# Kernel optimization log

Measured on AMD Instinct MI355X. Metric: run time of the kernel, lower is better.

Reference implementation:

```python
import jax, jax.numpy as jnp
import numpy as np

B, T, U, H, M, K, C = 64, 800, 80, 512, 20, 10, 80  # batch, tsteps, char len, rnn_size, nmixtures, kmixtures, char_vec_len


def _lstm(x, W, Uw, b):
    """Keras-semantics LSTM (gate order i,f,g,o), zero initial state. x: [B,T,D] -> [B,T,H]."""
    xg = jnp.einsum('btd,dh->bth', x, W) + b  # precompute input contribution
    h0 = jnp.zeros((x.shape[0], Uw.shape[0]), x.dtype)
    c0 = jnp.zeros_like(h0)

    def step(carry, zt):
        h, c = carry
        z = zt + h @ Uw
        i, f, g, o = jnp.split(z, 4, axis=-1)
        c = jax.nn.sigmoid(f) * c + jax.nn.sigmoid(i) * jnp.tanh(g)
        h = jax.nn.sigmoid(o) * jnp.tanh(c)
        return (h, c), h

    _, hs = jax.lax.scan(step, (h0, c0), jnp.swapaxes(xg, 0, 1))
    return jnp.swapaxes(hs, 0, 1)


def _forward(stroke_data, char_seq, kappa0, W0, U0, b0, W1, U1, b1, W2, U2, b2, Wa, ba, Wm, bm):
    lstm0_out = _lstm(stroke_data, W0, U0, b0)  # [B,T,H]
    # Attention window: the per-timestep loop in the source only carries kappa,
    # which is a running sum of exp(kappa_offset) -> vectorize via cumsum.
    abk = jnp.exp(jnp.einsum('bth,hk->btk', lstm0_out, Wa) + ba)  # [B,T,3K]
    alpha, beta, koff = jnpp_split = jnp.split(abk, 3, axis=-1)
    kappa = kappa0[:, None, :, 0] + jnp.cumsum(koff, axis=1)  # [B,T,K]
    u = jnp.arange(char_seq.shape[1], dtype=stroke_data.dtype)  # [U]
    # phi: [B,T,U] = sum_k alpha * exp(-beta * (kappa - u)^2)
    phi = jnp.sum(alpha[..., None] * jnp.exp(-beta[..., None] * (kappa[..., None] - u) ** 2), axis=2)
    windows = jnp.einsum('btu,buc->btc', phi, char_seq)  # [B,T,C]
    aug = jnp.concatenate([lstm0_out, windows, stroke_data], axis=-1)
    lstm1_out = _lstm(aug, W1, U1, b1)
    lstm2_out = _lstm(lstm1_out, W2, U2, b2)
    mdn = jnp.einsum('bth,hn->btn', lstm2_out, Wm) + bm  # [B,T,1+6M]
    eos_hat = mdn[..., 0:1]
    pi_hat, mu1, mu2, s1_hat, s2_hat, rho_hat = jnp.split(mdn[..., 1:], 6, axis=-1)
    return jnp.concatenate([
        jax.nn.sigmoid(-eos_hat),
        jax.nn.softmax(pi_hat, axis=-1),
        mu1, mu2,
        jnp.exp(s1_hat), jnp.exp(s2_hat),
        jnp.tanh(rho_hat),
    ], axis=-1)  # [B,T,1+6M]


def setup_inputs() -> dict:
    key = jax.random.key(0)
    ks = jax.random.split(key, 12)
    init = lambda k, shape: jax.random.truncated_normal(k, -2.0, 2.0, shape, jnp.float32) * 0.075
    return {
        'stroke_data': jax.random.normal(ks[0], (B, T, 3), jnp.float32),
        'char_seq': jax.nn.one_hot(jax.random.randint(ks[1], (B, U), 0, C), C, dtype=jnp.float32),
        'kappa0': jnp.zeros((B, K, 1), jnp.float32),
        'W0': init(ks[2], (3, 4 * H)), 'U0': init(ks[3], (H, 4 * H)), 'b0': jnp.zeros((4 * H,)),
        'W1': init(ks[4], (H + C + 3, 4 * H)), 'U1': init(ks[5], (H, 4 * H)), 'b1': jnp.zeros((4 * H,)),
        'W2': init(ks[6], (H, 4 * H)), 'U2': init(ks[7], (H, 4 * H)), 'b2': jnp.zeros((4 * H,)),
        'Wa': init(ks[8], (H, 3 * K)),
        'ba': -3.0 + 0.25 * jax.random.truncated_normal(ks[9], -2.0, 2.0, (3 * K,), jnp.float32),
        'Wm': init(ks[10], (H, 1 + 6 * M)), 'bm': jnp.zeros((1 + 6 * M,)),
    }


def reference(stroke_data, char_seq, kappa0, W0, U0, b0, W1, U1, b1, W2, U2, b2, Wa, ba, Wm, bm):
    return _forward(stroke_data, char_seq, kappa0, W0, U0, b0, W1, U1, b1, W2, U2, b2, Wa, ba, Wm, bm)
```

## Files before the change

kernel.cpp:

```cpp
#include <hip/hip_runtime.h>

typedef unsigned short u16;
typedef unsigned int u32;
typedef short v8s __attribute__((ext_vector_type(8)));
typedef float v4f __attribute__((ext_vector_type(4)));
typedef unsigned int v4u __attribute__((ext_vector_type(4)));
typedef unsigned int v2u __attribute__((ext_vector_type(2)));

#define MFMA16 __builtin_amdgcn_mfma_f32_16x16x32_bf16

constexpr int TT = 800;
constexpr int NBLK = 178;

constexpr int AUGB  = 2240;
constexpr int AUG2B = 2048;

constexpr size_t AUGR_OFF  = 131072;
constexpr size_t AUG2R_OFF = AUGR_OFF + (size_t)4 * 64 * AUGB;
constexpr size_t WAT_OFF   = AUG2R_OFF + (size_t)4 * 64 * AUG2B;
constexpr size_t WS_ZERO   = WAT_OFF + (size_t)32 * 512 * 2;

constexpr u32 SMEM_BYTES = 82944;

enum { G_S0D = 0, G_SAD = 1, G_S1D = 2, G_S2D = 3, G_S1R = 4, G_SAR = 5, G_S2R = 6, G_SMR = 7 };

__device__ __forceinline__ float bf2f(u16 u) { return __uint_as_float(((u32)u) << 16); }
__device__ __forceinline__ u16 f2bf(float f) {
    u32 x = __float_as_uint(f);
    return (u16)((x + 0x7fffu + ((x >> 16) & 1u)) >> 16);
}
__device__ __forceinline__ short f2bfs(float f) { return (short)f2bf(f); }
__device__ __forceinline__ float sigf(float x) { return 1.f / (1.f + __expf(-x)); }
__device__ __forceinline__ float tanhf2(float x) { return 1.f - 2.f / (1.f + __expf(2.f * x)); }

__device__ __forceinline__ __amdgpu_buffer_rsrc_t mkrsrc(const void* p) {
    return __builtin_amdgcn_make_buffer_rsrc((void*)p, (short)0, -1, 0x00020000);
}
__device__ __forceinline__ v4u ldu4(__amdgpu_buffer_rsrc_t r, int off) {
    return __builtin_amdgcn_raw_buffer_load_b128(r, off, 0, 17);
}
__device__ __forceinline__ void stq8(__amdgpu_buffer_rsrc_t r, int off, u16 a, u16 b, u16 c, u16 d) {
    v2u t; t[0] = (u32)a | ((u32)b << 16); t[1] = (u32)c | ((u32)d << 16);
    __builtin_amdgcn_raw_buffer_store_b64(t, r, off, 0, 17);
}
__device__ __forceinline__ void stq4(__amdgpu_buffer_rsrc_t r, int off, u16 a, u16 b) {
    u32 t = (u32)a | ((u32)b << 16);
    __builtin_amdgcn_raw_buffer_store_b32(t, r, off, 0, 17);
}

__device__ __forceinline__ void publish(u32* ctrl, int g, int t, int blk) {
    __hip_atomic_fetch_add(ctrl + g * 4096 + (t & 3) * 1024 + (blk & 15) * 64, 1u,
                           __ATOMIC_RELAXED, __HIP_MEMORY_SCOPE_AGENT);
}
__device__ __forceinline__ void wait4(u32* ctrl,
    int g0, int t0, u32 n0, int g1, int t1, u32 n1,
    int g2, int t2, u32 n2, int g3, int t3, u32 n3)
{
    if (threadIdx.x < 64) {
        const int lane = threadIdx.x;
        const int cl = lane >> 4, k = lane & 15;
        int g, tt; u32 nn;
        if (cl == 0)      { g = g0; tt = t0; nn = n0; }
        else if (cl == 1) { g = g1; tt = t1; nn = n1; }
        else if (cl == 2) { g = g2; tt = t2; nn = n2; }
        else              { g = g3; tt = t3; nn = n3; }
        const u32 tgt = (g >= 0 && tt >= 0) ? nn * (u32)((tt >> 2) + 1) : 0u;
        u32* p = (tgt > 0) ? (ctrl + g * 4096 + (tt & 3) * 1024 + k * 64) : (u32*)0;
        int sp = 0;
        for (;;) {
            u32 v = p ? __hip_atomic_load(p, __ATOMIC_RELAXED, __HIP_MEMORY_SCOPE_AGENT) : 0u;
            v += __shfl_xor(v, 1); v += __shfl_xor(v, 2);
            v += __shfl_xor(v, 4); v += __shfl_xor(v, 8);
            const bool bad = (tgt > 0) && (v < tgt);
            if (__ballot(bad) == 0ull) break;
            if (sp >= 2) __builtin_amdgcn_s_sleep(4);
            else if (sp == 1) __builtin_amdgcn_s_sleep(1);
            sp++;
        }
    }
    __syncthreads();
}

__global__ void wat_init(const float* __restrict__ Wa, u16* __restrict__ WaT) {
    __amdgpu_buffer_rsrc_t r = mkrsrc(WaT);
    for (int idx = blockIdx.x * 256 + threadIdx.x; idx < 32 * 512 / 2; idx += gridDim.x * 256) {
        const int e0 = idx * 2, e1 = e0 + 1;
        const int n0 = e0 >> 9, k0 = e0 & 511;
        const int n1 = e1 >> 9, k1 = e1 & 511;
        const u16 a = (n0 < 30) ? f2bf(Wa[k0 * 30 + n0]) : (u16)0;
        const u16 b = (n1 < 30) ? f2bf(Wa[k1 * 30 + n1]) : (u16)0;
        stq4(r, idx * 4, a, b);
    }
}

__global__ __launch_bounds__(256, 1) void hw_main(
    const float* __restrict__ stroke, const float* __restrict__ charseq, const float* __restrict__ kappa0,
    const float* __restrict__ W0, const float* __restrict__ U0, const float* __restrict__ b0,
    const float* __restrict__ W1, const float* __restrict__ U1, const float* __restrict__ b1,
    const float* __restrict__ W2, const float* __restrict__ U2, const float* __restrict__ b2,
    const float* __restrict__ ba, const float* __restrict__ Wm, const float* __restrict__ bm,
    float* __restrict__ out, char* __restrict__ ws)
{
    extern __shared__ __align__(16) char smem[];
    u32* ctrl = (u32*)ws;
    u16* augr  = (u16*)(ws + AUGR_OFF);
    u16* aug2r = (u16*)(ws + AUG2R_OFF);
    const u16* WaT = (const u16*)(ws + WAT_OFF);

    const int blk = blockIdx.x, tid = threadIdx.x;
    const int wave = tid >> 6, lane = tid & 63;
    const int quad = lane >> 4, l15 = lane & 15;

    if (blk < 32) {
        const int cs = blk & 15, mg = blk >> 4;
        __amdgpu_buffer_rsrc_t ra = mkrsrc(augr);
        u16*   aL  = (u16*)smem;
        float* zb  = (float*)(smem + 33280);
        float* w0s = (float*)(smem + 50176);
        float* b0s = (float*)(smem + 51712);
        if (tid < 128) {
            const int cn2 = (tid >> 5) * 512 + cs * 32 + (tid & 31);
            b0s[tid] = b0[cn2];
            #pragma unroll
            for (int d = 0; d < 3; d++) w0s[d * 128 + tid] = W0[d * 2048 + cn2];
        }
        v8s bw0[16], bw1[16];
        {
            const int cnA = wave * 512 + cs * 32 + l15;
            const int cnB = cnA + 16;
            #pragma unroll
            for (int kc = 0; kc < 16; kc++)
                #pragma unroll
                for (int j = 0; j < 8; j++) {
                    const int k = kc * 32 + quad * 8 + j;
                    bw0[kc][j] = f2bfs(U0[k * 2048 + cnA]);
                    bw1[kc][j] = f2bfs(U0[k * 2048 + cnB]);
                }
        }
        float cst[4] = {0.f, 0.f, 0.f, 0.f};
        __syncthreads();
        #pragma unroll 1
        for (int t = 0; t < TT; t++) {
            wait4(ctrl, G_S0D, t - 1, 32, G_S1R, t - 4, 64, G_SAR, t - 4, 16, -1, 0, 0);
            {
                const int base = (((t + 3) & 3) * 64 + mg * 32) * AUGB;
                #pragma unroll
                for (int c8 = 0; c8 < 8; c8++) {
                    const int c = tid + 256 * c8;
                    const int row = c >> 6, off = c & 63;
                    v4u d = ldu4(ra, base + row * AUGB + off * 16);
                    *(v4u*)((char*)aL + row * 1040 + off * 16) = d;
                }
            }
            __syncthreads();
            v4f c0a = {0,0,0,0}, c0b = {0,0,0,0}, c1a = {0,0,0,0}, c1b = {0,0,0,0};
            const int xo = quad * 16;
            #pragma unroll
            for (int kc = 0; kc < 16; kc++) {
                v8s x0 = *(const v8s*)((const char*)aL + l15 * 1040 + kc * 64 + xo);
                v8s x1 = *(const v8s*)((const char*)aL + (16 + l15) * 1040 + kc * 64 + xo);
                c0a = MFMA16(x0, bw0[kc], c0a, 0, 0, 0);
                c1a = MFMA16(x0, bw1[kc], c1a, 0, 0, 0);
                c0b = MFMA16(x1, bw0[kc], c0b, 0, 0, 0);
                c1b = MFMA16(x1, bw1[kc], c1b, 0, 0, 0);
            }
            const int n0 = wave * 32 + l15, n1 = n0 + 16;
            #pragma unroll
            for (int r = 0; r < 4; r++) {
                zb[(quad * 4 + r) * 132 + n0] = c0a[r];
                zb[(quad * 4 + r) * 132 + n1] = c1a[r];
                zb[(16 + quad * 4 + r) * 132 + n0] = c0b[r];
                zb[(16 + quad * 4 + r) * 132 + n1] = c1b[r];
            }
            __syncthreads();
            {
                const int bl = tid & 31, jj = tid >> 5;
                const int b = mg * 32 + bl;
                const float xx0 = stroke[(b * TT + t) * 3 + 0];
                const float xx1 = stroke[(b * TT + t) * 3 + 1];
                const float xx2 = stroke[(b * TT + t) * 3 + 2];
                u16 hv[4];
                #pragma unroll
                for (int m = 0; m < 4; m++) {
                    const int j = jj * 4 + m;
                    float z[4];
                    #pragma unroll
                    for (int g = 0; g < 4; g++) {
                        const int n = g * 32 + j;
                        z[g] = zb[bl * 132 + n] + b0s[n] + xx0 * w0s[n] + xx1 * w0s[128 + n] + xx2 * w0s[256 + n];
                    }
                    const float cc = sigf(z[1]) * cst[m] + sigf(z[0]) * tanhf2(z[2]);
                    cst[m] = cc;
                    hv[m] = f2bf(sigf(z[3]) * tanhf2(cc));
                }
                stq8(ra, ((t & 3) * 64 + b) * AUGB + (cs * 32 + jj * 4) * 2, hv[0], hv[1], hv[2], hv[3]);
            }
            __syncthreads();
            if (tid == 0) publish(ctrl, G_S0D, t, blk);
        }
    } else if (blk < 96) {
        const int q = blk - 32, cs = q >> 1, mg = q & 1;
        __amdgpu_buffer_rsrc_t ra = mkrsrc(augr);
        __amdgpu_buffer_rsrc_t r2 = mkrsrc(aug2r);
        u16*   aL  = (u16*)smem;
        float* zb  = (float*)(smem + 72192);
        float* b1s = (float*)(smem + 80896);
        if (tid < 64) b1s[tid] = b1[(tid >> 4) * 512 + cs * 16 + (tid & 15)];
        v8s bw[35];
        {
            const int cn = wave * 512 + cs * 16 + l15;
            #pragma unroll
            for (int kc = 0; kc < 35; kc++)
                #pragma unroll
                for (int j = 0; j < 8; j++) {
                    const int k = kc * 32 + quad * 8 + j;
                    short v = 0;
                    if (k < 595) v = f2bfs(W1[k * 2048 + cn]);
                    else if (k >= 596 && k < 1108) v = f2bfs(U1[(k - 596) * 2048 + cn]);
                    bw[kc][j] = v;
                }
        }
        float cst[2] = {0.f, 0.f};
        __syncthreads();
        #pragma unroll 1
        for (int t = 0; t < TT; t++) {
            wait4(ctrl, G_S0D, t, 32, G_SAD, t, 16, G_S1D, t - 1, 64, G_S2R, t - 4, 64);
            {
                const int base = ((t & 3) * 64 + mg * 32) * AUGB;
                #pragma unroll
                for (int c18 = 0; c18 < 18; c18++) {
                    const int c = tid + 256 * c18;
                    if (c < 4480) {
                        const int row = c / 140, off = c - row * 140;
                        v4u d = ldu4(ra, base + row * AUGB + off * 16);
                        *(v4u*)((char*)aL + row * 2256 + off * 16) = d;
                    }
                }
            }
            __syncthreads();
            if (tid == 0) publish(ctrl, G_S1R, t, blk);
            v4f c0 = {0,0,0,0}, c1 = {0,0,0,0};
            const int xo = quad * 16;
            #pragma unroll
            for (int kc = 0; kc < 35; kc++) {
                v8s x0 = *(const v8s*)((const char*)aL + l15 * 2256 + kc * 64 + xo);
                v8s x1 = *(const v8s*)((const char*)aL + (16 + l15) * 2256 + kc * 64 + xo);
                c0 = MFMA16(x0, bw[kc], c0, 0, 0, 0);
                c1 = MFMA16(x1, bw[kc], c1, 0, 0, 0);
            }
            #pragma unroll
            for (int r = 0; r < 4; r++) {
                zb[(quad * 4 + r) * 68 + wave * 17 + l15] = c0[r];
                zb[(16 + quad * 4 + r) * 68 + wave * 17 + l15] = c1[r];
            }
            __syncthreads();
            {
                const int bl = tid & 31, jj = tid >> 5;
                const int b = mg * 32 + bl;
                u16 hv[2];
                #pragma unroll
                for (int m = 0; m < 2; m++) {
                    const int j = jj * 2 + m;
                    float z[4];
                    #pragma unroll
                    for (int g = 0; g < 4; g++)
                        z[g] = zb[bl * 68 + g * 17 + j] + b1s[g * 16 + j];
                    const float cc = sigf(z[1]) * cst[m] + sigf(z[0]) * tanhf2(z[2]);
                    cst[m] = cc;
                    hv[m] = f2bf(sigf(z[3]) * tanhf2(cc));
                }
                stq4(ra, (((t + 1) & 3) * 64 + b) * AUGB + (596 + cs * 16 + jj * 2) * 2, hv[0], hv[1]);
                stq4(r2, ((t & 3) * 64 + b) * AUG2B + (cs * 16 + jj * 2) * 2, hv[0], hv[1]);
            }
            __syncthreads();
            if (tid == 0) publish(ctrl, G_S1D, t, blk);
        }
    } else if (blk < 160) {
        const int q = blk - 96, cs = q >> 1, mg = q & 1;
        __amdgpu_buffer_rsrc_t r2 = mkrsrc(aug2r);
        u16*   aL  = (u16*)smem;
        float* zb  = (float*)(smem + 66048);
        float* b2s = (float*)(smem + 74752);
        if (tid < 64) b2s[tid] = b2[(tid >> 4) * 512 + cs * 16 + (tid & 15)];
        v8s bw[32];
        {
            const int cn = wave * 512 + cs * 16 + l15;
            #pragma unroll
            for (int kc = 0; kc < 32; kc++)
                #pragma unroll
                for (int j = 0; j < 8; j++) {
                    const int k = kc * 32 + quad * 8 + j;
                    bw[kc][j] = (k < 512) ? f2bfs(W2[k * 2048 + cn]) : f2bfs(U2[(k - 512) * 2048 + cn]);
                }
        }
        float cst[2] = {0.f, 0.f};
        __syncthreads();
        #pragma unroll 1
        for (int t = 0; t < TT; t++) {
            wait4(ctrl, G_S1D, t, 64, G_S2D, t - 1, 64, G_SMR, t - 4, 2, -1, 0, 0);
            {
                const int base = ((t & 3) * 64 + mg * 32) * AUG2B;
                #pragma unroll
                for (int c16 = 0; c16 < 16; c16++) {
                    const int c = tid + 256 * c16;
                    const int row = c >> 7, off = c & 127;
                    v4u d = ldu4(r2, base + row * AUG2B + off * 16);
                    *(v4u*)((char*)aL + row * 2064 + off * 16) = d;
                }
            }
            __syncthreads();
            if (tid == 0) publish(ctrl, G_S2R, t, blk);
            v4f c0 = {0,0,0,0}, c1 = {0,0,0,0};
            const int xo = quad * 16;
            #pragma unroll
            for (int kc = 0; kc < 32; kc++) {
                v8s x0 = *(const v8s*)((const char*)aL + l15 * 2064 + kc * 64 + xo);
                v8s x1 = *(const v8s*)((const char*)aL + (16 + l15) * 2064 + kc * 64 + xo);
                c0 = MFMA16(x0, bw[kc], c0, 0, 0, 0);
                c1 = MFMA16(x1, bw[kc], c1, 0, 0, 0);
            }
            #pragma unroll
            for (int r = 0; r < 4; r++) {
                zb[(quad * 4 + r) * 68 + wave * 17 + l15] = c0[r];
                zb[(16 + quad * 4 + r) * 68 + wave * 17 + l15] = c1[r];
            }
            __syncthreads();
            {
                const int bl = tid & 31, jj = tid >> 5;
                const int b = mg * 32 + bl;
                u16 hv[2];
                #pragma unroll
                for (int m = 0; m < 2; m++) {
                    const int j = jj * 2 + m;
                    float z[4];
                    #pragma unroll
                    for (int g = 0; g < 4; g++)
                        z[g] = zb[bl * 68 + g * 17 + j] + b2s[g * 16 + j];
                    const float cc = sigf(z[1]) * cst[m] + sigf(z[0]) * tanhf2(z[2]);
                    cst[m] = cc;
                    hv[m] = f2bf(sigf(z[3]) * tanhf2(cc));
                }
                stq4(r2, (((t + 1) & 3) * 64 + b) * AUG2B + (512 + cs * 16 + jj * 2) * 2, hv[0], hv[1]);
            }
            __syncthreads();
            if (tid == 0) publish(ctrl, G_S2D, t, blk);
        }
    } else if (blk < 176) {
        const int a = blk - 160;
        const int b = a * 4 + wave;
        __amdgpu_buffer_rsrc_t ra = mkrsrc(augr);
        u16*   watl = (u16*)smem;
        u16*   hrow = (u16*)(smem + 33280);
        float* phis = (float*)(smem + 37440);
        u16*   idxs = (u16*)(smem + 38720);
        {
            #pragma unroll
            for (int c8 = 0; c8 < 8; c8++) {
                const int c = tid + 256 * c8;
                const int row = c >> 6, off = c & 63;
                *(v4u*)((char*)watl + row * 1040 + off * 16) = *(const v4u*)(WaT + row * 512 + off * 8);
            }
        }
        #pragma unroll
        for (int rep = 0; rep < 2; rep++) {
            const int u = rep * 64 + lane;
            if (u < 80) {
                int c = 0;
                #pragma unroll 1
                for (int cc = 0; cc < 80; cc++)
                    if (charseq[b * 6400 + u * 80 + cc] > 0.5f) c = cc;
                idxs[wave * 80 + u] = (u16)c;
            }
        }
        float kap = (lane < 10) ? kappa0[b * 10 + lane] : 0.f;
        const float baf = (lane < 30) ? ba[lane] : 0.f;
        const int nn = lane & 31;
        const int k0 = (lane >> 5) * 256;
        const u16* wrow = watl + nn * 520 + k0;
        __syncthreads();
        #pragma unroll 1
        for (int t = 0; t < TT; t++) {
            wait4(ctrl, G_S0D, t, 32, G_S1R, t - 4, 64, -1, 0, 0, -1, 0, 0);
            {
                const int row = tid >> 6, off = tid & 63;
                v4u d = ldu4(ra, ((t & 3) * 64 + a * 4 + row) * AUGB + off * 16);
                *(v4u*)((char*)hrow + row * 1040 + off * 16) = d;
            }
            __syncthreads();
            if (tid == 0) publish(ctrl, G_SAR, t, blk);
            float acc = 0.f;
            #pragma unroll
            for (int kk = 0; kk < 32; kk++) {
                v8s hv = *(const v8s*)((const char*)hrow + wave * 1040 + (k0 + kk * 8) * 2);
                v8s wv = *(const v8s*)(wrow + kk * 8);
                #pragma unroll
                for (int e = 0; e < 8; e++) acc += bf2f((u16)hv[e]) * bf2f((u16)wv[e]);
            }
            acc += __shfl_xor(acc, 32);
            const float abk = __expf(acc + baf);
            const float kofv = __shfl(abk, 20 + (lane < 10 ? lane : 0));
            if (lane < 10) kap += kofv;
            const float u1f = (float)lane;
            float p1 = 0.f, p2 = 0.f;
            #pragma unroll
            for (int kk = 0; kk < 10; kk++) {
                const float al = __shfl(abk, kk);
                const float be = __shfl(abk, 10 + kk);
                const float kp = __shfl(kap, kk);
                const float d1 = kp - u1f, d2 = kp - (u1f + 64.f);
                p1 += al * __expf(-be * d1 * d1);
                p2 += al * __expf(-be * d2 * d2);
            }
            phis[wave * 80 + lane] = p1;
            if (lane < 16) phis[wave * 80 + 64 + lane] = p2;
            __syncthreads();
            const int db = (((t & 3) * 64 + b) * AUGB) + 512 * 2;
            if (lane < 40) {
                const int c0 = 2 * lane;
                float w0 = 0.f, w1 = 0.f;
                #pragma unroll 1
                for (int u = 0; u < 80; u++) {
                    const float pv = phis[wave * 80 + u];
                    const int ix = (int)idxs[wave * 80 + u];
                    w0 += (ix == c0)     ? pv : 0.f;
                    w1 += (ix == c0 + 1) ? pv : 0.f;
                }
                stq4(ra, db + c0 * 2, f2bf(w0), f2bf(w1));
            } else if (lane == 40) {
                stq4(ra, db + 80 * 2, f2bf(stroke[(b * TT + t) * 3 + 0]), f2bf(stroke[(b * TT + t) * 3 + 1]));
            } else if (lane == 41) {
                stq4(ra, db + 82 * 2, f2bf(stroke[(b * TT + t) * 3 + 2]), (u16)0);
            }
            __syncthreads();
            if (tid == 0) publish(ctrl, G_SAD, t, blk);
        }
    } else {
        const int mgs = blk - 176;
        __amdgpu_buffer_rsrc_t r2 = mkrsrc(aug2r);
        u16*   aL = (u16*)smem;
        float* zb = (float*)(smem + 33280);
        v8s bw0[16], bw1[16];
        {
            const int nA = wave * 32 + l15, nB = nA + 16;
            #pragma unroll
            for (int kc = 0; kc < 16; kc++)
                #pragma unroll
                for (int j = 0; j < 8; j++) {
                    const int k = kc * 32 + quad * 8 + j;
                    bw0[kc][j] = (nA < 121) ? f2bfs(Wm[k * 121 + nA]) : (short)0;
                    bw1[kc][j] = (nB < 121) ? f2bfs(Wm[k * 121 + nB]) : (short)0;
                }
        }
        __syncthreads();
        #pragma unroll 1
        for (int t = 0; t < TT; t++) {
            wait4(ctrl, G_S2D, t, 64, -1, 0, 0, -1, 0, 0, -1, 0, 0);
            {
                const int base = (((t + 1) & 3) * 64 + mgs * 32) * AUG2B + 1024;
                #pragma unroll
                for (int c8 = 0; c8 < 8; c8++) {
                    const int c = tid + 256 * c8;
                    const int row = c >> 6, off = c & 63;
                    v4u d = ldu4(r2, base + row * AUG2B + off * 16);
                    *(v4u*)((char*)aL + row * 1040 + off * 16) = d;
                }
            }
            __syncthreads();
            if (tid == 0) publish(ctrl, G_SMR, t, blk);
            v4f c0a = {0,0,0,0}, c0b = {0,0,0,0}, c1a = {0,0,0,0}, c1b = {0,0,0,0};
            const int xo = quad * 16;
            #pragma unroll
            for (int kc = 0; kc < 16; kc++) {
                v8s x0 = *(const v8s*)((const char*)aL + l15 * 1040 + kc * 64 + xo);
                v8s x1 = *(const v8s*)((const char*)aL + (16 + l15) * 1040 + kc * 64 + xo);
                c0a = MFMA16(x0, bw0[kc], c0a, 0, 0, 0);
                c1a = MFMA16(x0, bw1[kc], c1a, 0, 0, 0);
                c0b = MFMA16(x1, bw0[kc], c0b, 0, 0, 0);
                c1b = MFMA16(x1, bw1[kc], c1b, 0, 0, 0);
            }
            const int n0 = wave * 32 + l15, n1 = n0 + 16;
            #pragma unroll
            for (int r = 0; r < 4; r++) {
                zb[(quad * 4 + r) * 132 + n0] = c0a[r];
                zb[(quad * 4 + r) * 132 + n1] = c1a[r];
                zb[(16 + quad * 4 + r) * 132 + n0] = c0b[r];
                zb[(16 + quad * 4 + r) * 132 + n1] = c1b[r];
            }
            __syncthreads();
            {
                const int b8 = tid >> 3, g8 = tid & 7;
                const int b = mgs * 32 + b8;
                const float* zr = zb + b8 * 132;
                float* orow = out + ((size_t)(b * TT + t)) * 121;
                if (g8 == 0) {
                    orow[0] = sigf(-(zr[0] + bm[0]));
                    float mx = -1e30f;
                    float zv[20];
                    #pragma unroll 1
                    for (int nl = 1; nl <= 20; nl++) { zv[nl - 1] = zr[nl] + bm[nl]; mx = fmaxf(mx, zv[nl - 1]); }
                    float ss = 0.f;
                    #pragma unroll 1
                    for (int nl = 0; nl < 20; nl++) { zv[nl] = __expf(zv[nl] - mx); ss += zv[nl]; }
                    const float inv = 1.f / ss;
                    #pragma unroll 1
                    for (int nl = 0; nl < 20; nl++) orow[nl + 1] = zv[nl] * inv;
                } else if (g8 <= 2) {
                    const int s0 = 21 + (g8 - 1) * 20;
                    #pragma unroll 1
                    for (int nl = s0; nl < s0 + 20; nl++) orow[nl] = zr[nl] + bm[nl];
                } else if (g8 <= 4) {
                    const int s0 = 61 + (g8 - 3) * 20;
                    #pragma unroll 1
                    for (int nl = s0; nl < s0 + 20; nl++) orow[nl] = __expf(zr[nl] + bm[nl]);
                } else if (g8 <= 6) {
                    const int s0 = 101 + (g8 - 5) * 10;
                    #pragma unroll 1
                    for (int nl = s0; nl < s0 + 10; nl++) orow[nl] = tanhf2(zr[nl] + bm[nl]);
                }
            }
            __syncthreads();
        }
    }
}

extern "C" void kernel_launch(void* const* d_in, const int* in_sizes, int n_in,
                              void* d_out, int out_size, void* d_ws, size_t ws_size,
                              hipStream_t stream) {
    const float* stroke  = (const float*)d_in[0];
    const float* charseq = (const float*)d_in[1];
    const float* kappa0  = (const float*)d_in[2];
    const float* W0 = (const float*)d_in[3];
    const float* U0 = (const float*)d_in[4];
    const float* b0 = (const float*)d_in[5];
    const float* W1 = (const float*)d_in[6];
    const float* U1 = (const float*)d_in[7];
    const float* b1 = (const float*)d_in[8];
    const float* W2 = (const float*)d_in[9];
    const float* U2 = (const float*)d_in[10];
    const float* b2 = (const float*)d_in[11];
    const float* Wa = (const float*)d_in[12];
    const float* ba = (const float*)d_in[13];
    const float* Wm = (const float*)d_in[14];
    const float* bm = (const float*)d_in[15];
    char* ws = (char*)d_ws;

    static bool attr_done = false;
    if (!attr_done) {
        hipFuncSetAttribute((const void*)hw_main,
                            hipFuncAttributeMaxDynamicSharedMemorySize, SMEM_BYTES);
        attr_done = true;
    }

    hipMemsetAsync(d_ws, 0, WS_ZERO, stream);
    wat_init<<<8, 256, 0, stream>>>(Wa, (u16*)(ws + WAT_OFF));
    hw_main<<<NBLK, 256, SMEM_BYTES, stream>>>(stroke, charseq, kappa0, W0, U0, b0,
                                               W1, U1, b1, W2, U2, b2, ba, Wm, bm,
                                               (float*)d_out, ws);
}
```

Baseline: 8.759 ms.

## Merge pairs of persistent blocks into 512-thread blocks, halving grid size

Each persistent role block now runs 8 waves instead of 4 and owns twice as many gate columns (or both batch halves for the MDN stage), so the grid shrinks from 178 to 89 blocks. This halves the number of blocks that publish and poll the inter-block step counters, which is meant to cut synchronization latency per timestep. In exchange each block does more LDS staging and the intra-block barriers cover twice the waves. The __launch_bounds__(512,2) hint may also limit registers for the large weight-resident register arrays and cause spills.

Result: slower. 9.900 ms (+13.0%).

```diff
diff --git a/kernel.cpp b/kernel.cpp
--- a/kernel.cpp
+++ b/kernel.cpp
@@ -10,7 +10,7 @@
 #define MFMA16 __builtin_amdgcn_mfma_f32_16x16x32_bf16
 
 constexpr int TT = 800;
-constexpr int NBLK = 178;
+constexpr int NBLK = 89;
 
 constexpr int AUGB  = 2240;
 constexpr int AUG2B = 2048;
@@ -20,7 +20,7 @@
 constexpr size_t WAT_OFF   = AUG2R_OFF + (size_t)4 * 64 * AUG2B;
 constexpr size_t WS_ZERO   = WAT_OFF + (size_t)32 * 512 * 2;
 
-constexpr u32 SMEM_BYTES = 82944;
+constexpr u32 SMEM_BYTES = 100352;
 
 enum { G_S0D = 0, G_SAD = 1, G_S1D = 2, G_S2D = 3, G_S1R = 4, G_SAR = 5, G_S2R = 6, G_SMR = 7 };
 
@@ -93,7 +93,7 @@
     }
 }
 
-__global__ __launch_bounds__(256, 1) void hw_main(
+__global__ __launch_bounds__(512, 2) void hw_main(
     const float* __restrict__ stroke, const float* __restrict__ charseq, const float* __restrict__ kappa0,
     const float* __restrict__ W0, const float* __restrict__ U0, const float* __restrict__ b0,
     const float* __restrict__ W1, const float* __restrict__ U1, const float* __restrict__ b1,
@@ -111,22 +111,24 @@
     const int wave = tid >> 6, lane = tid & 63;
     const int quad = lane >> 4, l15 = lane & 15;
 
-    if (blk < 32) {
-        const int cs = blk & 15, mg = blk >> 4;
+    if (blk < 16) {
+        const int cs = blk & 7, mg = blk >> 3;
+        const int gw = wave & 3, sw = wave >> 2;
         __amdgpu_buffer_rsrc_t ra = mkrsrc(augr);
         u16*   aL  = (u16*)smem;
         float* zb  = (float*)(smem + 33280);
-        float* w0s = (float*)(smem + 50176);
-        float* b0s = (float*)(smem + 51712);
-        if (tid < 128) {
-            const int cn2 = (tid >> 5) * 512 + cs * 32 + (tid & 31);
+        float* w0s = (float*)(smem + 66560);
+        float* b0s = (float*)(smem + 69632);
+        if (tid < 256) {
+            const int gg = tid >> 6, j = tid & 63;
+            const int cn2 = gg * 512 + cs * 64 + j;
             b0s[tid] = b0[cn2];
             #pragma unroll
-            for (int d = 0; d < 3; d++) w0s[d * 128 + tid] = W0[d * 2048 + cn2];
+            for (int d = 0; d < 3; d++) w0s[d * 256 + tid] = W0[d * 2048 + cn2];
         }
         v8s bw0[16], bw1[16];
         {
-            const int cnA = wave * 512 + cs * 32 + l15;
+            const int cnA = gw * 512 + cs * 64 + sw * 32 + l15;
             const int cnB = cnA + 16;
             #pragma unroll
             for (int kc = 0; kc < 16; kc++)
@@ -141,12 +143,12 @@
         __syncthreads();
         #pragma unroll 1
         for (int t = 0; t < TT; t++) {
-            wait4(ctrl, G_S0D, t - 1, 32, G_S1R, t - 4, 64, G_SAR, t - 4, 16, -1, 0, 0);
+            wait4(ctrl, G_S0D, t - 1, 16, G_S1R, t - 4, 32, G_SAR, t - 4, 8, -1, 0, 0);
             {
                 const int base = (((t + 3) & 3) * 64 + mg * 32) * AUGB;
                 #pragma unroll
-                for (int c8 = 0; c8 < 8; c8++) {
-                    const int c = tid + 256 * c8;
+                for (int c4 = 0; c4 < 4; c4++) {
+                    const int c = tid + 512 * c4;
                     const int row = c >> 6, off = c & 63;
                     v4u d = ldu4(ra, base + row * AUGB + off * 16);
                     *(v4u*)((char*)aL + row * 1040 + off * 16) = d;
@@ -167,10 +169,10 @@
             const int n0 = wave * 32 + l15, n1 = n0 + 16;
             #pragma unroll
             for (int r = 0; r < 4; r++) {
-                zb[(quad * 4 + r) * 132 + n0] = c0a[r];
-                zb[(quad * 4 + r) * 132 + n1] = c1a[r];
-                zb[(16 + quad * 4 + r) * 132 + n0] = c0b[r];
-                zb[(16 + quad * 4 + r) * 132 + n1] = c1b[r];
+                zb[(quad * 4 + r) * 260 + n0] = c0a[r];
+                zb[(quad * 4 + r) * 260 + n1] = c1a[r];
+                zb[(16 + quad * 4 + r) * 260 + n0] = c0b[r];
+                zb[(16 + quad * 4 + r) * 260 + n1] = c1b[r];
             }
             __syncthreads();
             {
@@ -185,30 +187,33 @@
                     const int j = jj * 4 + m;
                     float z[4];
                     #pragma unroll
-                    for (int g = 0; g < 4; g++) {
-                        const int n = g * 32 + j;
-                        z[g] = zb[bl * 132 + n] + b0s[n] + xx0 * w0s[n] + xx1 * w0s[128 + n] + xx2 * w0s[256 + n];
+                    for (int gg = 0; gg < 4; gg++) {
+                        const int zn = ((j >> 5) * 4 + gg) * 32 + (j & 31);
+                        const int nb = gg * 64 + j;
+                        z[gg] = zb[bl * 260 + zn] + b0s[nb]
+                              + xx0 * w0s[nb] + xx1 * w0s[256 + nb] + xx2 * w0s[512 + nb];
                     }
                     const float cc = sigf(z[1]) * cst[m] + sigf(z[0]) * tanhf2(z[2]);
                     cst[m] = cc;
                     hv[m] = f2bf(sigf(z[3]) * tanhf2(cc));
                 }
-                stq8(ra, ((t & 3) * 64 + b) * AUGB + (cs * 32 + jj * 4) * 2, hv[0], hv[1], hv[2], hv[3]);
+                stq8(ra, ((t & 3) * 64 + b) * AUGB + (cs * 64 + jj * 4) * 2, hv[0], hv[1], hv[2], hv[3]);
             }
             __syncthreads();
             if (tid == 0) publish(ctrl, G_S0D, t, blk);
         }
-    } else if (blk < 96) {
-        const int q = blk - 32, cs = q >> 1, mg = q & 1;
+    } else if (blk < 48) {
+        const int q = blk - 16, cs = q >> 1, mg = q & 1;
+        const int gw = wave & 3, sw = wave >> 2;
         __amdgpu_buffer_rsrc_t ra = mkrsrc(augr);
         __amdgpu_buffer_rsrc_t r2 = mkrsrc(aug2r);
         u16*   aL  = (u16*)smem;
         float* zb  = (float*)(smem + 72192);
-        float* b1s = (float*)(smem + 80896);
-        if (tid < 64) b1s[tid] = b1[(tid >> 4) * 512 + cs * 16 + (tid & 15)];
+        float* b1s = (float*)(smem + 90112);
+        if (tid < 128) b1s[tid] = b1[(tid >> 5) * 512 + cs * 32 + (tid & 31)];
         v8s bw[35];
         {
-            const int cn = wave * 512 + cs * 16 + l15;
+            const int cn = gw * 512 + cs * 32 + sw * 16 + l15;
             #pragma unroll
             for (int kc = 0; kc < 35; kc++)
                 #pragma unroll
@@ -224,12 +229,12 @@
         __syncthreads();
         #pragma unroll 1
         for (int t = 0; t < TT; t++) {
-            wait4(ctrl, G_S0D, t, 32, G_SAD, t, 16, G_S1D, t - 1, 64, G_S2R, t - 4, 64);
+            wait4(ctrl, G_S0D, t, 16, G_SAD, t, 8, G_S1D, t - 1, 32, G_S2R, t - 4, 32);
             {
                 const int base = ((t & 3) * 64 + mg * 32) * AUGB;
                 #pragma unroll
-                for (int c18 = 0; c18 < 18; c18++) {
-                    const int c = tid + 256 * c18;
+                for (int c9 = 0; c9 < 9; c9++) {
+                    const int c = tid + 512 * c9;
                     if (c < 4480) {
                         const int row = c / 140, off = c - row * 140;
                         v4u d = ldu4(ra, base + row * AUGB + off * 16);
@@ -250,8 +255,8 @@
             }
             #pragma unroll
             for (int r = 0; r < 4; r++) {
-                zb[(quad * 4 + r) * 68 + wave * 17 + l15] = c0[r];
-                zb[(16 + quad * 4 + r) * 68 + wave * 17 + l15] = c1[r];
+                zb[(quad * 4 + r) * 140 + wave * 17 + l15] = c0[r];
+                zb[(16 + quad * 4 + r) * 140 + wave * 17 + l15] = c1[r];
             }
             __syncthreads();
             {
@@ -263,28 +268,29 @@
                     const int j = jj * 2 + m;
                     float z[4];
                     #pragma unroll
-                    for (int g = 0; g < 4; g++)
-                        z[g] = zb[bl * 68 + g * 17 + j] + b1s[g * 16 + j];
+                    for (int gg = 0; gg < 4; gg++)
+                        z[gg] = zb[bl * 140 + ((j >> 4) * 4 + gg) * 17 + (j & 15)] + b1s[gg * 32 + j];
                     const float cc = sigf(z[1]) * cst[m] + sigf(z[0]) * tanhf2(z[2]);
                     cst[m] = cc;
                     hv[m] = f2bf(sigf(z[3]) * tanhf2(cc));
                 }
-                stq4(ra, (((t + 1) & 3) * 64 + b) * AUGB + (596 + cs * 16 + jj * 2) * 2, hv[0], hv[1]);
-                stq4(r2, ((t & 3) * 64 + b) * AUG2B + (cs * 16 + jj * 2) * 2, hv[0], hv[1]);
+                stq4(ra, (((t + 1) & 3) * 64 + b) * AUGB + (596 + cs * 32 + jj * 2) * 2, hv[0], hv[1]);
+                stq4(r2, ((t & 3) * 64 + b) * AUG2B + (cs * 32 + jj * 2) * 2, hv[0], hv[1]);
             }
             __syncthreads();
             if (tid == 0) publish(ctrl, G_S1D, t, blk);
         }
-    } else if (blk < 160) {
-        const int q = blk - 96, cs = q >> 1, mg = q & 1;
+    } else if (blk < 80) {
+        const int q = blk - 48, cs = q >> 1, mg = q & 1;
+        const int gw = wave & 3, sw = wave >> 2;
         __amdgpu_buffer_rsrc_t r2 = mkrsrc(aug2r);
         u16*   aL  = (u16*)smem;
         float* zb  = (float*)(smem + 66048);
-        float* b2s = (float*)(smem + 74752);
-        if (tid < 64) b2s[tid] = b2[(tid >> 4) * 512 + cs * 16 + (tid & 15)];
+        float* b2s = (float*)(smem + 83968);
+        if (tid < 128) b2s[tid] = b2[(tid >> 5) * 512 + cs * 32 + (tid & 31)];
         v8s bw[32];
         {
-            const int cn = wave * 512 + cs * 16 + l15;
+            const int cn = gw * 512 + cs * 32 + sw * 16 + l15;
             #pragma unroll
             for (int kc = 0; kc < 32; kc++)
                 #pragma unroll
@@ -297,12 +303,12 @@
         __syncthreads();
         #pragma unroll 1
         for (int t = 0; t < TT; t++) {
-            wait4(ctrl, G_S1D, t, 64, G_S2D, t - 1, 64, G_SMR, t - 4, 2, -1, 0, 0);
+            wait4(ctrl, G_S1D, t, 32, G_S2D, t - 1, 32, G_SMR, t - 4, 1, -1, 0, 0);
             {
                 const int base = ((t & 3) * 64 + mg * 32) * AUG2B;
                 #pragma unroll
-                for (int c16 = 0; c16 < 16; c16++) {
-                    const int c = tid + 256 * c16;
+                for (int c8 = 0; c8 < 8; c8++) {
+                    const int c = tid + 512 * c8;
                     const int row = c >> 7, off = c & 127;
                     v4u d = ldu4(r2, base + row * AUG2B + off * 16);
                     *(v4u*)((char*)aL + row * 2064 + off * 16) = d;
@@ -321,8 +327,8 @@
             }
             #pragma unroll
             for (int r = 0; r < 4; r++) {
-                zb[(quad * 4 + r) * 68 + wave * 17 + l15] = c0[r];
-                zb[(16 + quad * 4 + r) * 68 + wave * 17 + l15] = c1[r];
+                zb[(quad * 4 + r) * 140 + wave * 17 + l15] = c0[r];
+                zb[(16 + quad * 4 + r) * 140 + wave * 17 + l15] = c1[r];
             }
             __syncthreads();
             {
@@ -334,29 +340,29 @@
                     const int j = jj * 2 + m;
                     float z[4];
                     #pragma unroll
-                    for (int g = 0; g < 4; g++)
-                        z[g] = zb[bl * 68 + g * 17 + j] + b2s[g * 16 + j];
+                    for (int gg = 0; gg < 4; gg++)
+                        z[gg] = zb[bl * 140 + ((j >> 4) * 4 + gg) * 17 + (j & 15)] + b2s[gg * 32 + j];
                     const float cc = sigf(z[1]) * cst[m] + sigf(z[0]) * tanhf2(z[2]);
                     cst[m] = cc;
                     hv[m] = f2bf(sigf(z[3]) * tanhf2(cc));
                 }
-                stq4(r2, (((t + 1) & 3) * 64 + b) * AUG2B + (512 + cs * 16 + jj * 2) * 2, hv[0], hv[1]);
+                stq4(r2, (((t + 1) & 3) * 64 + b) * AUG2B + (512 + cs * 32 + jj * 2) * 2, hv[0], hv[1]);
             }
             __syncthreads();
             if (tid == 0) publish(ctrl, G_S2D, t, blk);
         }
-    } else if (blk < 176) {
-        const int a = blk - 160;
-        const int b = a * 4 + wave;
+    } else if (blk < 88) {
+        const int a = blk - 80;
+        const int b = a * 8 + wave;
         __amdgpu_buffer_rsrc_t ra = mkrsrc(augr);
         u16*   watl = (u16*)smem;
         u16*   hrow = (u16*)(smem + 33280);
-        float* phis = (float*)(smem + 37440);
-        u16*   idxs = (u16*)(smem + 38720);
+        float* phis = (float*)(smem + 41600);
+        u16*   idxs = (u16*)(smem + 44160);
         {
             #pragma unroll
-            for (int c8 = 0; c8 < 8; c8++) {
-                const int c = tid + 256 * c8;
+            for (int c4 = 0; c4 < 4; c4++) {
+                const int c = tid + 512 * c4;
                 const int row = c >> 6, off = c & 63;
                 *(v4u*)((char*)watl + row * 1040 + off * 16) = *(const v4u*)(WaT + row * 512 + off * 8);
             }
@@ -380,10 +386,10 @@
         __syncthreads();
         #pragma unroll 1
         for (int t = 0; t < TT; t++) {
-            wait4(ctrl, G_S0D, t, 32, G_S1R, t - 4, 64, -1, 0, 0, -1, 0, 0);
+            wait4(ctrl, G_S0D, t, 16, G_S1R, t - 4, 32, -1, 0, 0, -1, 0, 0);
             {
                 const int row = tid >> 6, off = tid & 63;
-                v4u d = ldu4(ra, ((t & 3) * 64 + a * 4 + row) * AUGB + off * 16);
+                v4u d = ldu4(ra, ((t & 3) * 64 + a * 8 + row) * AUGB + off * 16);
                 *(v4u*)((char*)hrow + row * 1040 + off * 16) = d;
             }
             __syncthreads();
@@ -435,13 +441,13 @@
             if (tid == 0) publish(ctrl, G_SAD, t, blk);
         }
     } else {
-        const int mgs = blk - 176;
+        const int mgs = wave >> 2, wv = wave & 3;
         __amdgpu_buffer_rsrc_t r2 = mkrsrc(aug2r);
         u16*   aL = (u16*)smem;
-        float* zb = (float*)(smem + 33280);
+        float* zb = (float*)(smem + 66560);
         v8s bw0[16], bw1[16];
         {
-            const int nA = wave * 32 + l15, nB = nA + 16;
+            const int nA = wv * 32 + l15, nB = nA + 16;
             #pragma unroll
             for (int kc = 0; kc < 16; kc++)
                 #pragma unroll
@@ -454,12 +460,12 @@
         __syncthreads();
         #pragma unroll 1
         for (int t = 0; t < TT; t++) {
-            wait4(ctrl, G_S2D, t, 64, -1, 0, 0, -1, 0, 0, -1, 0, 0);
-            {
-                const int base = (((t + 1) & 3) * 64 + mgs * 32) * AUG2B + 1024;
+            wait4(ctrl, G_S2D, t, 32, -1, 0, 0, -1, 0, 0, -1, 0, 0);
+            {
+                const int base = (((t + 1) & 3) * 64) * AUG2B + 1024;
                 #pragma unroll
                 for (int c8 = 0; c8 < 8; c8++) {
-                    const int c = tid + 256 * c8;
+                    const int c = tid + 512 * c8;
                     const int row = c >> 6, off = c & 63;
                     v4u d = ldu4(r2, base + row * AUG2B + off * 16);
                     *(v4u*)((char*)aL + row * 1040 + off * 16) = d;
@@ -471,25 +477,25 @@
             const int xo = quad * 16;
             #pragma unroll
             for (int kc = 0; kc < 16; kc++) {
-                v8s x0 = *(const v8s*)((const char*)aL + l15 * 1040 + kc * 64 + xo);
-                v8s x1 = *(const v8s*)((const char*)aL + (16 + l15) * 1040 + kc * 64 + xo);
+                v8s x0 = *(const v8s*)((const char*)aL + (mgs * 32 + l15) * 1040 + kc * 64 + xo);
+                v8s x1 = *(const v8s*)((const char*)aL + (mgs * 32 + 16 + l15) * 1040 + kc * 64 + xo);
                 c0a = MFMA16(x0, bw0[kc], c0a, 0, 0, 0);
                 c1a = MFMA16(x0, bw1[kc], c1a, 0, 0, 0);
                 c0b = MFMA16(x1, bw0[kc], c0b, 0, 0, 0);
                 c1b = MFMA16(x1, bw1[kc], c1b, 0, 0, 0);
             }
-            const int n0 = wave * 32 + l15, n1 = n0 + 16;
+            const int n0 = wv * 32 + l15, n1 = n0 + 16;
             #pragma unroll
             for (int r = 0; r < 4; r++) {
-                zb[(quad * 4 + r) * 132 + n0] = c0a[r];
-                zb[(quad * 4 + r) * 132 + n1] = c1a[r];
-                zb[(16 + quad * 4 + r) * 132 + n0] = c0b[r];
-                zb[(16 + quad * 4 + r) * 132 + n1] = c1b[r];
+                zb[(mgs * 32 + quad * 4 + r) * 132 + n0] = c0a[r];
+                zb[(mgs * 32 + quad * 4 + r) * 132 + n1] = c1a[r];
+                zb[(mgs * 32 + 16 + quad * 4 + r) * 132 + n0] = c0b[r];
+                zb[(mgs * 32 + 16 + quad * 4 + r) * 132 + n1] = c1b[r];
             }
             __syncthreads();
             {
                 const int b8 = tid >> 3, g8 = tid & 7;
-                const int b = mgs * 32 + b8;
+                const int b = b8;
                 const float* zr = zb + b8 * 132;
                 float* orow = out + ((size_t)(b * TT + t)) * 121;
                 if (g8 == 0) {
@@ -553,7 +559,7 @@
 
     hipMemsetAsync(d_ws, 0, WS_ZERO, stream);
     wat_init<<<8, 256, 0, stream>>>(Wa, (u16*)(ws + WAT_OFF));
-    hw_main<<<NBLK, 256, SMEM_BYTES, stream>>>(stroke, charseq, kappa0, W0, U0, b0,
+    hw_main<<<NBLK, 512, SMEM_BYTES, stream>>>(stroke, charseq, kappa0, W0, U0, b0,
                                                W1, U1, b1, W2, U2, b2, ba, Wm, bm,
                                                (float*)d_out, ws);
 }
```

## Split LSTM input waits per batch-half and overlap input-part MFMA with recurrent wait

Applied to the files above, without the earlier changes.

Synchronisation counters are now partitioned by batch half (mb offset), so each stage waits only on producers for its own 32-row batch group instead of all blocks. LSTM1 and LSTM2 blocks first load and multiply the input (lower-layer) part of their concatenated input, then wait on the previous-step recurrent hidden state before loading and multiplying the recurrent half. This moves the recurrent dependency later in each step. Stroke loads are hoisted ahead of the wait. The cost is an extra wait and barrier per step, and a risk of miscounting if the per-half counter targets are wrong.

Result: no change. 8.748 ms (-0.1%).

```diff
diff --git a/kernel.cpp b/kernel.cpp
--- a/kernel.cpp
+++ b/kernel.cpp
@@ -39,6 +39,9 @@
 __device__ __forceinline__ v4u ldu4(__amdgpu_buffer_rsrc_t r, int off) {
     return __builtin_amdgcn_raw_buffer_load_b128(r, off, 0, 17);
 }
+__device__ __forceinline__ v2u ldu8(__amdgpu_buffer_rsrc_t r, int off) {
+    return __builtin_amdgcn_raw_buffer_load_b64(r, off, 0, 17);
+}
 __device__ __forceinline__ void stq8(__amdgpu_buffer_rsrc_t r, int off, u16 a, u16 b, u16 c, u16 d) {
     v2u t; t[0] = (u32)a | ((u32)b << 16); t[1] = (u32)c | ((u32)d << 16);
     __builtin_amdgcn_raw_buffer_store_b64(t, r, off, 0, 17);
@@ -48,24 +51,24 @@
     __builtin_amdgcn_raw_buffer_store_b32(t, r, off, 0, 17);
 }
 
-__device__ __forceinline__ void publish(u32* ctrl, int g, int t, int blk) {
-    __hip_atomic_fetch_add(ctrl + g * 4096 + (t & 3) * 1024 + (blk & 15) * 64, 1u,
+__device__ __forceinline__ void publish(u32* ctrl, int g, int t, int sub) {
+    __hip_atomic_fetch_add(ctrl + g * 4096 + (t & 3) * 1024 + (sub & 15) * 64, 1u,
                            __ATOMIC_RELAXED, __HIP_MEMORY_SCOPE_AGENT);
 }
 __device__ __forceinline__ void wait4(u32* ctrl,
-    int g0, int t0, u32 n0, int g1, int t1, u32 n1,
-    int g2, int t2, u32 n2, int g3, int t3, u32 n3)
+    int g0, int t0, u32 n0, int m0, int g1, int t1, u32 n1, int m1,
+    int g2, int t2, u32 n2, int m2, int g3, int t3, u32 n3, int m3)
 {
     if (threadIdx.x < 64) {
         const int lane = threadIdx.x;
         const int cl = lane >> 4, k = lane & 15;
-        int g, tt; u32 nn;
-        if (cl == 0)      { g = g0; tt = t0; nn = n0; }
-        else if (cl == 1) { g = g1; tt = t1; nn = n1; }
-        else if (cl == 2) { g = g2; tt = t2; nn = n2; }
-        else              { g = g3; tt = t3; nn = n3; }
+        int g, tt, mb; u32 nn;
+        if (cl == 0)      { g = g0; tt = t0; nn = n0; mb = m0; }
+        else if (cl == 1) { g = g1; tt = t1; nn = n1; mb = m1; }
+        else if (cl == 2) { g = g2; tt = t2; nn = n2; mb = m2; }
+        else              { g = g3; tt = t3; nn = n3; mb = m3; }
         const u32 tgt = (g >= 0 && tt >= 0) ? nn * (u32)((tt >> 2) + 1) : 0u;
-        u32* p = (tgt > 0) ? (ctrl + g * 4096 + (tt & 3) * 1024 + k * 64) : (u32*)0;
+        u32* p = (tgt > 0) ? (ctrl + g * 4096 + (tt & 3) * 1024 + (mb + (k & 7)) * 64) : (u32*)0;
         int sp = 0;
         for (;;) {
             u32 v = p ? __hip_atomic_load(p, __ATOMIC_RELAXED, __HIP_MEMORY_SCOPE_AGENT) : 0u;
@@ -113,6 +116,7 @@
 
     if (blk < 32) {
         const int cs = blk & 15, mg = blk >> 4;
+        const int mb = mg * 8, sub = mb + (cs & 7);
         __amdgpu_buffer_rsrc_t ra = mkrsrc(augr);
         u16*   aL  = (u16*)smem;
         float* zb  = (float*)(smem + 33280);
@@ -138,10 +142,15 @@
                 }
         }
         float cst[4] = {0.f, 0.f, 0.f, 0.f};
+        const int bl_ = tid & 31;
+        const int bpre = mg * 32 + bl_;
         __syncthreads();
         #pragma unroll 1
         for (int t = 0; t < TT; t++) {
-            wait4(ctrl, G_S0D, t - 1, 32, G_S1R, t - 4, 64, G_SAR, t - 4, 16, -1, 0, 0);
+            const float xx0 = stroke[(bpre * TT + t) * 3 + 0];
+            const float xx1 = stroke[(bpre * TT + t) * 3 + 1];
+            const float xx2 = stroke[(bpre * TT + t) * 3 + 2];
+            wait4(ctrl, G_S0D, t - 1, 32, mb, G_S1R, t - 4, 64, mb, G_SAR, t - 4, 16, mb, -1, 0, 0, 0);
             {
                 const int base = (((t + 3) & 3) * 64 + mg * 32) * AUGB;
                 #pragma unroll
@@ -176,9 +185,6 @@
             {
                 const int bl = tid & 31, jj = tid >> 5;
                 const int b = mg * 32 + bl;
-                const float xx0 = stroke[(b * TT + t) * 3 + 0];
-                const float xx1 = stroke[(b * TT + t) * 3 + 1];
-                const float xx2 = stroke[(b * TT + t) * 3 + 2];
                 u16 hv[4];
                 #pragma unroll
                 for (int m = 0; m < 4; m++) {
@@ -196,10 +202,11 @@
                 stq8(ra, ((t & 3) * 64 + b) * AUGB + (cs * 32 + jj * 4) * 2, hv[0], hv[1], hv[2], hv[3]);
             }
             __syncthreads();
-            if (tid == 0) publish(ctrl, G_S0D, t, blk);
+            if (tid == 0) publish(ctrl, G_S0D, t, sub);
         }
     } else if (blk < 96) {
         const int q = blk - 32, cs = q >> 1, mg = q & 1;
+        const int mb = mg * 8, sub = mb + (cs & 7);
         __amdgpu_buffer_rsrc_t ra = mkrsrc(augr);
         __amdgpu_buffer_rsrc_t r2 = mkrsrc(aug2r);
         u16*   aL  = (u16*)smem;
@@ -220,29 +227,53 @@
                     bw[kc][j] = v;
                 }
         }
+        if (tid < 32) { v4u z4 = {0,0,0,0}; *(v4u*)((char*)aL + tid * 2256 + 2224) = z4; }
         float cst[2] = {0.f, 0.f};
         __syncthreads();
         #pragma unroll 1
         for (int t = 0; t < TT; t++) {
-            wait4(ctrl, G_S0D, t, 32, G_SAD, t, 16, G_S1D, t - 1, 64, G_S2R, t - 4, 64);
+            wait4(ctrl, G_S0D, t, 32, mb, G_SAD, t, 16, mb, G_S2R, t - 4, 64, mb, -1, 0, 0, 0);
             {
                 const int base = ((t & 3) * 64 + mg * 32) * AUGB;
                 #pragma unroll
-                for (int c18 = 0; c18 < 18; c18++) {
-                    const int c = tid + 256 * c18;
-                    if (c < 4480) {
-                        const int row = c / 140, off = c - row * 140;
+                for (int c10 = 0; c10 < 10; c10++) {
+                    const int c = tid + 256 * c10;
+                    if (c < 2400) {
+                        const int row = c / 75, off = c - row * 75;
                         v4u d = ldu4(ra, base + row * AUGB + off * 16);
                         *(v4u*)((char*)aL + row * 2256 + off * 16) = d;
                     }
                 }
             }
             __syncthreads();
-            if (tid == 0) publish(ctrl, G_S1R, t, blk);
+            if (tid == 0) publish(ctrl, G_S1R, t, sub);
+            wait4(ctrl, G_S1D, t - 1, 64, mb, -1, 0, 0, 0, -1, 0, 0, 0, -1, 0, 0, 0);
+            {
+                const int base = ((t & 3) * 64 + mg * 32) * AUGB;
+                if (tid < 32) {
+                    v2u d8 = ldu8(ra, base + tid * AUGB + 1192);
+                    *(v2u*)((char*)aL + tid * 2256 + 1192) = d8;
+                }
+                #pragma unroll
+                for (int c8 = 0; c8 < 8; c8++) {
+                    const int c = tid + 256 * c8;
+                    const int row = c >> 6, off = 75 + (c & 63);
+                    v4u d = ldu4(ra, base + row * AUGB + off * 16);
+                    *(v4u*)((char*)aL + row * 2256 + off * 16) = d;
+                }
+            }
             v4f c0 = {0,0,0,0}, c1 = {0,0,0,0};
             const int xo = quad * 16;
             #pragma unroll
-            for (int kc = 0; kc < 35; kc++) {
+            for (int kc = 0; kc < 18; kc++) {
+                v8s x0 = *(const v8s*)((const char*)aL + l15 * 2256 + kc * 64 + xo);
+                v8s x1 = *(const v8s*)((const char*)aL + (16 + l15) * 2256 + kc * 64 + xo);
+                c0 = MFMA16(x0, bw[kc], c0, 0, 0, 0);
+                c1 = MFMA16(x1, bw[kc], c1, 0, 0, 0);
+            }
+            __syncthreads();
+            #pragma unroll
+            for (int kc = 18; kc < 35; kc++) {
                 v8s x0 = *(const v8s*)((const char*)aL + l15 * 2256 + kc * 64 + xo);
                 v8s x1 = *(const v8s*)((const char*)aL + (16 + l15) * 2256 + kc * 64 + xo);
                 c0 = MFMA16(x0, bw[kc], c0, 0, 0, 0);
@@ -273,10 +304,11 @@
                 stq4(r2, ((t & 3) * 64 + b) * AUG2B + (cs * 16 + jj * 2) * 2, hv[0], hv[1]);
             }
             __syncthreads();
-            if (tid == 0) publish(ctrl, G_S1D, t, blk);
+            if (tid == 0) publish(ctrl, G_S1D, t, sub);
         }
     } else if (blk < 160) {
         const int q = blk - 96, cs = q >> 1, mg = q & 1;
+        const int mb = mg * 8, sub = mb + (cs & 7);
         __amdgpu_buffer_rsrc_t r2 = mkrsrc(aug2r);
         u16*   aL  = (u16*)smem;
         float* zb  = (float*)(smem + 66048);
@@ -297,23 +329,42 @@
         __syncthreads();
         #pragma unroll 1
         for (int t = 0; t < TT; t++) {
-            wait4(ctrl, G_S1D, t, 64, G_S2D, t - 1, 64, G_SMR, t - 4, 2, -1, 0, 0);
+            wait4(ctrl, G_S1D, t, 64, mb, G_SMR, t - 4, 2, mb, -1, 0, 0, 0, -1, 0, 0, 0);
             {
                 const int base = ((t & 3) * 64 + mg * 32) * AUG2B;
                 #pragma unroll
-                for (int c16 = 0; c16 < 16; c16++) {
-                    const int c = tid + 256 * c16;
-                    const int row = c >> 7, off = c & 127;
+                for (int c8 = 0; c8 < 8; c8++) {
+                    const int c = tid + 256 * c8;
+                    const int row = c >> 6, off = c & 63;
                     v4u d = ldu4(r2, base + row * AUG2B + off * 16);
                     *(v4u*)((char*)aL + row * 2064 + off * 16) = d;
                 }
             }
             __syncthreads();
-            if (tid == 0) publish(ctrl, G_S2R, t, blk);
+            if (tid == 0) publish(ctrl, G_S2R, t, sub);
+            wait4(ctrl, G_S2D, t - 1, 64, mb, -1, 0, 0, 0, -1, 0, 0, 0, -1, 0, 0, 0);
+            {
+                const int base = ((t & 3) * 64 + mg * 32) * AUG2B;
+                #pragma unroll
+                for (int c8 = 0; c8 < 8; c8++) {
+                    const int c = tid + 256 * c8;
+                    const int row = c >> 6, off = 64 + (c & 63);
+                    v4u d = ldu4(r2, base + row * AUG2B + off * 16);
+                    *(v4u*)((char*)aL + row * 2064 + off * 16) = d;
+                }
+            }
             v4f c0 = {0,0,0,0}, c1 = {0,0,0,0};
             const int xo = quad * 16;
             #pragma unroll
-            for (int kc = 0; kc < 32; kc++) {
+            for (int kc = 0; kc < 16; kc++) {
+                v8s x0 = *(const v8s*)((const char*)aL + l15 * 2064 + kc * 64 + xo);
+                v8s x1 = *(const v8s*)((const char*)aL + (16 + l15) * 2064 + kc * 64 + xo);
+                c0 = MFMA16(x0, bw[kc], c0, 0, 0, 0);
+                c1 = MFMA16(x1, bw[kc], c1, 0, 0, 0);
+            }
+            __syncthreads();
+            #pragma unroll
+            for (int kc = 16; kc < 32; kc++) {
                 v8s x0 = *(const v8s*)((const char*)aL + l15 * 2064 + kc * 64 + xo);
                 v8s x1 = *(const v8s*)((const char*)aL + (16 + l15) * 2064 + kc * 64 + xo);
                 c0 = MFMA16(x0, bw[kc], c0, 0, 0, 0);
@@ -343,10 +394,11 @@
                 stq4(r2, (((t + 1) & 3) * 64 + b) * AUG2B + (512 + cs * 16 + jj * 2) * 2, hv[0], hv[1]);
             }
             __syncthreads();
-            if (tid == 0) publish(ctrl, G_S2D, t, blk);
+            if (tid == 0) publish(ctrl, G_S2D, t, sub);
         }
     } else if (blk < 176) {
         const int a = blk - 160;
+        const int mg = a >> 3, mb = mg * 8, sub = mb + (a & 7);
         const int b = a * 4 + wave;
         __amdgpu_buffer_rsrc_t ra = mkrsrc(augr);
         u16*   watl = (u16*)smem;
@@ -380,14 +432,17 @@
         __syncthreads();
         #pragma unroll 1
         for (int t = 0; t < TT; t++) {
-            wait4(ctrl, G_S0D, t, 32, G_S1R, t - 4, 64, -1, 0, 0, -1, 0, 0);
+            float sx0 = 0.f, sx1 = 0.f;
+            if (lane == 40) { sx0 = stroke[(b * TT + t) * 3 + 0]; sx1 = stroke[(b * TT + t) * 3 + 1]; }
+            else if (lane == 41) { sx0 = stroke[(b * TT + t) * 3 + 2]; }
+            wait4(ctrl, G_S0D, t, 32, mb, G_S1R, t - 4, 64, mb, -1, 0, 0, 0, -1, 0, 0, 0);
             {
                 const int row = tid >> 6, off = tid & 63;
                 v4u d = ldu4(ra, ((t & 3) * 64 + a * 4 + row) * AUGB + off * 16);
                 *(v4u*)((char*)hrow + row * 1040 + off * 16) = d;
             }
             __syncthreads();
-            if (tid == 0) publish(ctrl, G_SAR, t, blk);
+            if (tid == 0) publish(ctrl, G_SAR, t, sub);
             float acc = 0.f;
             #pragma unroll
             for (int kk = 0; kk < 32; kk++) {
@@ -427,15 +482,16 @@
                 }
                 stq4(ra, db + c0 * 2, f2bf(w0), f2bf(w1));
             } else if (lane == 40) {
-                stq4(ra, db + 80 * 2, f2bf(stroke[(b * TT + t) * 3 + 0]), f2bf(stroke[(b * TT + t) * 3 + 1]));
+                stq4(ra, db + 80 * 2, f2bf(sx0), f2bf(sx1));
             } else if (lane == 41) {
-                stq4(ra, db + 82 * 2, f2bf(stroke[(b * TT + t) * 3 + 2]), (u16)0);
-            }
-            __syncthreads();
-            if (tid == 0) publish(ctrl, G_SAD, t, blk);
+                stq4(ra, db + 82 * 2, f2bf(sx0), (u16)0);
+            }
+            __syncthreads();
+            if (tid == 0) publish(ctrl, G_SAD, t, sub);
         }
     } else {
         const int mgs = blk - 176;
+        const int mb = mgs * 8, sub = mb;
         __amdgpu_buffer_rsrc_t r2 = mkrsrc(aug2r);
         u16*   aL = (u16*)smem;
         float* zb = (float*)(smem + 33280);
@@ -454,7 +510,7 @@
         __syncthreads();
         #pragma unroll 1
         for (int t = 0; t < TT; t++) {
-            wait4(ctrl, G_S2D, t, 64, -1, 0, 0, -1, 0, 0, -1, 0, 0);
+            wait4(ctrl, G_S2D, t, 64, mb, -1, 0, 0, 0, -1, 0, 0, 0, -1, 0, 0, 0);
             {
                 const int base = (((t + 1) & 3) * 64 + mgs * 32) * AUG2B + 1024;
                 #pragma unroll
@@ -466,7 +522,7 @@
                 }
             }
             __syncthreads();
-            if (tid == 0) publish(ctrl, G_SMR, t, blk);
+            if (tid == 0) publish(ctrl, G_SMR, t, sub);
             v4f c0a = {0,0,0,0}, c0b = {0,0,0,0}, c1a = {0,0,0,0}, c1b = {0,0,0,0};
             const int xo = quad * 16;
             #pragma unroll
```
